# Performance work log

Measured on AMD Instinct MI355X. Metric: run time of the kernel, lower is better.

## Reference

```python
import jax, jax.numpy as jnp
import numpy as np
import math

B, H, L, DK, D, LOCAL = 4, 8, 2048, 64, 512, 4


def setup_inputs() -> dict:
    key = jax.random.key(0)
    ks = jax.random.split(key, 9)
    n = L
    return {
        'query': jax.random.normal(ks[0], (B, H, L, DK), jnp.float32),
        'key': jax.random.normal(ks[1], (B, H, L, DK), jnp.float32),
        'value': jax.random.normal(ks[2], (B, H, L, DK), jnp.float32),
        'users': jax.random.normal(ks[3], (B, L, D), jnp.float32),
        'mask': jnp.tril(jnp.ones((L, L), dtype=bool))[None, None],  # causal [1,1,L,L]
        'rel_pos_w': jax.random.normal(ks[4], (2 * n - 1, DK * LOCAL), jnp.float32) * 0.02,
        'user_proj_w': jax.random.normal(ks[5], (DK * LOCAL, D), jnp.float32) * 0.02,
        'user_proj_b': jax.random.normal(ks[6], (DK * LOCAL,), jnp.float32) * 0.02,
        'mlp_w': jax.random.normal(ks[7], (LOCAL, DK), jnp.float32) * 0.1,
        'mlp_b': jax.random.normal(ks[8], (LOCAL,), jnp.float32) * 0.1,
    }


def reference(query, key, value, users, mask, rel_pos_w, user_proj_w, user_proj_b, mlp_w, mlp_b):
    b, h, l, dk = query.shape
    local = mlp_w.shape[0]
    g = h - local
    n = l
    scale = 1.0 / math.sqrt(dk)
    NEG = -1e12  # MAX_VAL in the torch source

    # ---- global heads: plain softmax attention ----
    qg, kg, vg = query[:, :g], key[:, :g], value[:, :g]
    sg = jnp.einsum('bhqd,bhkd->bhqk', qg, kg) * scale
    sg = jnp.where(mask, sg, NEG)
    pg = jax.nn.softmax(sg, axis=-1)
    og = jnp.einsum('bhqk,bhkd->bhqd', pg, vg)

    # ---- local (LOCKER) heads ----
    ql, kl, vl = query[:, g:], key[:, g:], value[:, g:]
    sl = jnp.einsum('bhqd,bhkd->bhqk', ql, kl) * scale

    # reweight = Linear(d_k,1)(rel_pos + v_q + v_k + user_proj(users)_q) per local head.
    # Linear over a sum decomposes exactly (same math, avoids [b,local,l,l,dk] tensor):
    rel_tab = rel_pos_w.reshape(2 * n - 1, local, dk)
    rel_scores = jnp.einsum('rhd,hd->rh', rel_tab, mlp_w)          # [2n-1, local]
    pos = jnp.arange(n)
    distance = pos[None, :] - pos[:, None] + n - 1                  # [l, l]
    rel_term = rel_scores[distance].transpose(2, 0, 1)              # [local, l, l]

    v_term = jnp.einsum('bhkd,hd->bhk', vl, mlp_w)                  # [b, local, l]
    u = (users @ user_proj_w.T + user_proj_b).reshape(b, l, local, dk)
    u_term = jnp.einsum('bqhd,hd->bhq', u, mlp_w)                   # [b, local, l]

    reweight = (rel_term[None]
                + v_term[:, :, None, :]      # value_l.unsqueeze(-3): varies over key idx
                + v_term[:, :, :, None]      # value_l.unsqueeze(-2): varies over query idx
                + u_term[:, :, :, None]      # user term broadcast over key idx
                + mlp_b[None, :, None, None])

    sl = sl + reweight
    sl = jnp.where(mask, sl, NEG)
    pl = jax.nn.softmax(sl, axis=-1)
    ol = jnp.einsum('bhqk,bhkd->bhqd', pl, vl)

    return jnp.concatenate([og, ol], axis=1)  # [b, h, l, d_k]
```

## Files before the change

kernel.cpp:

```cpp
#include <hip/hip_runtime.h>

#define TL 2048
#define NHEAD 8
#define NLOC 4
#define L2E 1.44269504f
#define PSTRIDE 4352

typedef __attribute__((ext_vector_type(4))) float f32x4;
typedef __attribute__((ext_vector_type(16))) float f32x16;
typedef __attribute__((ext_vector_type(8))) __bf16 bf16x8;
typedef __attribute__((ext_vector_type(8))) unsigned short u16x8;
typedef __attribute__((ext_vector_type(4))) unsigned int u32x4;

static __device__ __forceinline__ unsigned short f2bf(float f) {
    unsigned u = __float_as_uint(f);
    u = (u + 0x7FFFu + ((u >> 16) & 1u)) >> 16;
    return (unsigned short)u;
}
static __device__ __forceinline__ unsigned int cvtpk(float a, float b) {
    unsigned int w;
    asm("v_cvt_pk_bf16_f32 %0, %1, %2" : "=v"(w) : "v"(a), "v"(b));
    return w;
}
static __device__ __forceinline__ void gl_lds16(const void* g, void* l) {
    __builtin_amdgcn_global_load_lds(
        (const __attribute__((address_space(1))) void*)g,
        (__attribute__((address_space(3))) void*)l, 16, 0, 0);
}

__global__ __launch_bounds__(256) void preconv_kernel(
    const float* __restrict__ key, const float* __restrict__ value,
    const float* __restrict__ mlp_w, const float* __restrict__ rel_pos_w,
    unsigned short* __restrict__ Kb, unsigned short* __restrict__ Vtb,
    float* __restrict__ vtbf, float* __restrict__ rel_sf) {
    int blk = blockIdx.x;
    int t = threadIdx.x;
    int wave = t >> 6, lane = t & 63;

    if (blk >= 1024) {
        int r = (blk - 1024) * 4 + wave;
        if (r < 2 * TL - 1) {
#pragma unroll
            for (int hp = 0; hp < 4; ++hp) {
                float v = rel_pos_w[r * 256 + hp * 64 + lane] * mlp_w[hp * 64 + lane];
#pragma unroll
                for (int off = 32; off; off >>= 1) v += __shfl_xor(v, off);
                if (lane == 0) rel_sf[hp * 4096 + r] = v * L2E;
            }
        }
        return;
    }

    __shared__ float Vf[64][66];
    int bh = blk >> 5, kt = blk & 31;
    int h = bh & 7, b = bh >> 3;
    size_t src = (size_t)blk * 4096;
    size_t dst = (size_t)blk * 4096;

#pragma unroll
    for (int i = 0; i < 2; ++i) {
        int ch = t + i * 256;
        int row = ch >> 3, c = ch & 7;
        const float* kp = key + src + row * 64 + c * 8;
        f32x4 a = *(const f32x4*)kp;
        f32x4 bb = *(const f32x4*)(kp + 4);
        u16x8 o;
#pragma unroll
        for (int j = 0; j < 4; ++j) { o[j] = f2bf(a[j]); o[4 + j] = f2bf(bb[j]); }
        *(u16x8*)&Kb[dst + row * 64 + ((c ^ (row & 7)) << 3)] = o;
    }
    {
        int row = t >> 2, q4 = t & 3;
        const float* vp = value + src + row * 64 + q4 * 16;
#pragma unroll
        for (int j = 0; j < 4; ++j)
            *(f32x4*)&Vf[row][q4 * 16 + j * 4] = *(const f32x4*)(vp + j * 4);
    }
    __syncthreads();
#pragma unroll
    for (int i = 0; i < 2; ++i) {
        int ch = t + i * 256;
        int dr = ch >> 3, c = ch & 7;
        u16x8 o;
#pragma unroll
        for (int j = 0; j < 8; ++j) o[j] = f2bf(Vf[c * 8 + j][dr]);
        *(u16x8*)&Vtb[dst + dr * 64 + ((c ^ (dr & 7)) << 3)] = o;
    }
    if (h >= NLOC) {
        float mw = mlp_w[(h - NLOC) * 64 + lane];
        float* vout = vtbf + (size_t)((b * NLOC + h - NLOC) * TL) + kt * 64;
#pragma unroll
        for (int i = 0; i < 16; ++i) {
            int row = wave * 16 + i;
            float v = Vf[row][lane] * mw;
#pragma unroll
            for (int off = 32; off; off >>= 1) v += __shfl_xor(v, off);
            if (lane == 0) vout[row] = v * L2E;
        }
    }
}

#define MFMA32(A, B, C) __builtin_amdgcn_mfma_f32_32x32x16_bf16(A, B, C, 0, 0, 0)

__global__ __launch_bounds__(256, 4) void attn_kernel(
    const float* __restrict__ query,
    const unsigned short* __restrict__ Kb, const unsigned short* __restrict__ Vtb,
    const float* __restrict__ rel_sf, const float* __restrict__ vtbf,
    float* __restrict__ part) {

    __shared__ __align__(16) unsigned char smem[35328];
    unsigned short* Ks0 = (unsigned short*)smem;
    unsigned short* Vt0 = (unsigned short*)(smem + 16384);
    float* relw  = (float*)(smem + 32768);
    float* biasf = (float*)(smem + 34816);

    int bid = blockIdx.x;
    int bh = bid & 31;
    int sid = bid >> 5;
    int i = 0, s = 0, acc = 0;
#pragma unroll
    for (int ii = 15; ii >= 0; --ii) {
        int ns = (2 * ii + 7) / 6;
        if (sid >= acc && sid < acc + ns) { i = ii; s = sid - acc; }
        acc += ns;
    }
    int k_b = 6 * s;
    int k_e = min(6 * s + 6, 2 * i + 2);
    int q0 = i << 7;

    int h = bh & 7, b = bh >> 3;
    bool islocal = (h >= NLOC);
    int t = threadIdx.x;
    int w = t >> 6;
    int l31 = t & 31;
    int hi = (t >> 5) & 1;
    int sw = l31 & 7;
    int qrel = 32 * w + l31;
    int qglob = q0 + qrel;
    int qmaxw = q0 + 32 * w + 31;

    size_t tbase = (size_t)bh * 32 * 4096;
    const unsigned short* Ktiles = Kb + tbase;
    const unsigned short* Vtiles = Vtb + tbase;
    const float* vtpf = vtbf + (islocal ? (size_t)((b * NLOC + h - NLOC) * TL) : 0);
    int idxlo = 64 * k_b - q0 + 1920;
    const float* relsrc = rel_sf + (islocal ? ((h - NLOC) * 4096 + idxlo) : 0);

    gl_lds16(Ktiles + (size_t)k_b * 4096 + t * 8, Ks0 + t * 8);
    gl_lds16(Ktiles + (size_t)k_b * 4096 + 2048 + t * 8, Ks0 + 2048 + t * 8);
    gl_lds16(Vtiles + (size_t)k_b * 4096 + t * 8, Vt0 + t * 8);
    gl_lds16(Vtiles + (size_t)k_b * 4096 + 2048 + t * 8, Vt0 + 2048 + t * 8);
    if (islocal) {
        if (t < 128) *((f32x4*)relw + t) = *((const f32x4*)relsrc + t);
        if (t < 16) ((f32x4*)biasf)[t] = ((const f32x4*)(vtpf + (size_t)k_b * 64))[t];
    }

    const float SC = 0.125f * L2E;
    bf16x8 qf[4];
    {
        const float* qsrc = query + ((size_t)bh * TL + qglob) * 64 + 8 * hi;
#pragma unroll
        for (int mq = 0; mq < 4; ++mq) {
            f32x4 a = *(const f32x4*)(qsrc + 16 * mq);
            f32x4 c = *(const f32x4*)(qsrc + 16 * mq + 4);
            u16x8 u;
#pragma unroll
            for (int j = 0; j < 4; ++j) { u[j] = f2bf(a[j] * SC); u[4 + j] = f2bf(c[j] * SC); }
            qf[mq] = __builtin_bit_cast(bf16x8, u);
        }
    }

    float m = -1e30f, lsum = 0.f;
    f32x16 O0 = {0,0,0,0,0,0,0,0,0,0,0,0,0,0,0,0};
    f32x16 O1 = {0,0,0,0,0,0,0,0,0,0,0,0,0,0,0,0};

    __syncthreads();

    int cur = 0;
    for (int kt = k_b; kt < k_e; ++kt) {
        unsigned short* Ks = Ks0 + cur * 4096;
        unsigned short* Vt = Vt0 + cur * 4096;
        const float* bias = biasf + cur * 64;

        if (kt + 1 < k_e) {
            int nb = cur ^ 1;
            gl_lds16(Ktiles + (size_t)(kt + 1) * 4096 + t * 8, Ks0 + nb * 4096 + t * 8);
            gl_lds16(Ktiles + (size_t)(kt + 1) * 4096 + 2048 + t * 8, Ks0 + nb * 4096 + 2048 + t * 8);
            gl_lds16(Vtiles + (size_t)(kt + 1) * 4096 + t * 8, Vt0 + nb * 4096 + t * 8);
            gl_lds16(Vtiles + (size_t)(kt + 1) * 4096 + 2048 + t * 8, Vt0 + nb * 4096 + 2048 + t * 8);
            if (islocal && t < 16)
                ((f32x4*)(biasf + nb * 64))[t] =
                    ((const f32x4*)(vtpf + (size_t)(kt + 1) * 64))[t];
        }

        bool active = (64 * kt <= qmaxw);
        bool maskt = (64 * kt + 63 > q0 + 32 * w);
        if (active) {
#pragma unroll
            for (int h2 = 0; h2 < 2; ++h2) {
                f32x16 S = {0,0,0,0,0,0,0,0,0,0,0,0,0,0,0,0};
                __builtin_amdgcn_s_setprio(1);
#pragma unroll
                for (int mq = 0; mq < 4; ++mq) {
                    int ch = ((2 * mq + hi) ^ sw) << 3;
                    const bf16x8 kf = *(const bf16x8*)&Ks[(32 * h2 + l31) * 64 + ch];
                    S = MFMA32(kf, qf[mq], S);
                }
                __builtin_amdgcn_s_setprio(0);

                if (islocal) {
                    int rbase = 64 * (kt - k_b) + 32 * h2 + 4 * hi + 127 - qrel;
#pragma unroll
                    for (int g = 0; g < 4; ++g) {
                        int kk0 = 32 * h2 + 8 * g + 4 * hi;
                        f32x4 bv = *(const f32x4*)&bias[kk0];
#pragma unroll
                        for (int j = 0; j < 4; ++j)
                            S[4 * g + j] += bv[j] + relw[rbase + 8 * g + j];
                    }
                }
                if (maskt) {
                    int koff = 64 * kt + 32 * h2 + 4 * hi - qglob;
#pragma unroll
                    for (int r = 0; r < 16; ++r) {
                        int kk = (r & 3) + 8 * (r >> 2);
                        if (koff + kk > 0) S[r] = -1e30f;
                    }
                }
                float pmax = -1e30f;
#pragma unroll
                for (int r = 0; r < 16; ++r) pmax = fmaxf(pmax, S[r]);
                pmax = fmaxf(pmax, __shfl_xor(pmax, 32));
                if (__any(pmax > m + 11.5f)) {
                    float nm2 = fmaxf(m, pmax);
                    float corr = exp2f(m - nm2);
                    lsum *= corr;
#pragma unroll
                    for (int r = 0; r < 16; ++r) { O0[r] *= corr; O1[r] *= corr; }
                    m = nm2;
                }
                float ps = 0.f;
#pragma unroll
                for (int r = 0; r < 16; ++r) {
                    float p = exp2f(S[r] - m);
                    S[r] = p; ps += p;
                }
                ps += __shfl_xor(ps, 32);
                lsum += ps;

                __builtin_amdgcn_s_setprio(1);
#pragma unroll
                for (int kq = 0; kq < 2; ++kq) {
                    int ra = 8 * kq;
                    unsigned int x0 = cvtpk(S[ra + 0], S[ra + 1]);
                    unsigned int x1 = cvtpk(S[ra + 2], S[ra + 3]);
                    unsigned int y0 = cvtpk(S[ra + 4], S[ra + 5]);
                    unsigned int y1 = cvtpk(S[ra + 6], S[ra + 7]);
                    asm("v_permlane32_swap_b32 %0, %1" : "+v"(x0), "+v"(y0));
                    asm("v_permlane32_swap_b32 %0, %1" : "+v"(x1), "+v"(y1));
                    u32x4 fw;
                    fw[0] = x0; fw[1] = x1; fw[2] = y0; fw[3] = y1;
                    const bf16x8 pf = __builtin_bit_cast(bf16x8, fw);
                    int ch = ((4 * h2 + 2 * kq + hi) ^ sw) << 3;
                    const bf16x8 vf0 = *(const bf16x8*)&Vt[l31 * 64 + ch];
                    const bf16x8 vf1 = *(const bf16x8*)&Vt[(32 + l31) * 64 + ch];
                    O0 = MFMA32(vf0, pf, O0);
                    O1 = MFMA32(vf1, pf, O1);
                }
                __builtin_amdgcn_s_setprio(0);
            }
        }
        __syncthreads();
        cur ^= 1;
    }

    float* pp = part + (size_t)bid * PSTRIDE;
    unsigned int* po = (unsigned int*)pp;
#pragma unroll
    for (int g = 0; g < 4; ++g) {
        unsigned int w0 = cvtpk(O0[4 * g + 0], O0[4 * g + 1]);
        unsigned int w1 = cvtpk(O0[4 * g + 2], O0[4 * g + 3]);
        unsigned int w2 = cvtpk(O1[4 * g + 0], O1[4 * g + 1]);
        unsigned int w3 = cvtpk(O1[4 * g + 2], O1[4 * g + 3]);
        int dp0 = 4 * g + 2 * hi;
        po[dp0 * 128 + qrel] = w0;
        po[(dp0 + 1) * 128 + qrel] = w1;
        po[(16 + dp0) * 128 + qrel] = w2;
        po[(16 + dp0 + 1) * 128 + qrel] = w3;
    }
    if (hi == 0) { pp[4096 + qrel] = m; pp[4224 + qrel] = lsum; }
}

__global__ __launch_bounds__(128) void merge_kernel(
    const float* __restrict__ part, float* __restrict__ out) {
    __shared__ float sc[6][128];
    int bid = blockIdx.x;
    int bh = bid & 31, i = bid >> 5;
    int n = (2 * i + 7) / 6;
    int sb = 0;
    for (int ii = 15; ii > i; --ii) sb += (2 * ii + 7) / 6;
    int t = threadIdx.x;

    float mv[6], lv[6];
#pragma unroll
    for (int s2 = 0; s2 < 6; ++s2) {
        mv[s2] = -1e30f; lv[s2] = 0.f;
        if (s2 < n) {
            const float* pp = part + (size_t)((sb + s2) * 32 + bh) * PSTRIDE;
            mv[s2] = pp[4096 + t]; lv[s2] = pp[4224 + t];
        }
    }
    float nm = mv[0];
#pragma unroll
    for (int s2 = 1; s2 < 6; ++s2) nm = fmaxf(nm, mv[s2]);
    float den = 0.f;
    float cf[6];
#pragma unroll
    for (int s2 = 0; s2 < 6; ++s2) { cf[s2] = exp2f(mv[s2] - nm); den += lv[s2] * cf[s2]; }
    float inv = 1.0f / den;
#pragma unroll
    for (int s2 = 0; s2 < 6; ++s2) if (s2 < n) sc[s2][t] = cf[s2] * inv;
    __syncthreads();

    size_t obase = (size_t)bh * TL * 64 + (size_t)(128 * i + t) * 64;
    for (int seg = 0; seg < 4; ++seg) {
        float o[16];
#pragma unroll
        for (int j = 0; j < 16; ++j) o[j] = 0.f;
#pragma unroll
        for (int s2 = 0; s2 < 6; ++s2) {
            if (s2 < n) {
                const unsigned int* po =
                    (const unsigned int*)(part + (size_t)((sb + s2) * 32 + bh) * PSTRIDE);
                float wsc = sc[s2][t];
#pragma unroll
                for (int j = 0; j < 8; ++j) {
                    unsigned int wv = po[(seg * 8 + j) * 128 + t];
                    o[2 * j]     += wsc * __uint_as_float((wv & 0xffffu) << 16);
                    o[2 * j + 1] += wsc * __uint_as_float(wv & 0xffff0000u);
                }
            }
        }
#pragma unroll
        for (int c = 0; c < 4; ++c)
            *(f32x4*)(out + obase + seg * 16 + 4 * c) = *(const f32x4*)&o[4 * c];
    }
}

extern "C" void kernel_launch(void* const* d_in, const int* in_sizes, int n_in,
                              void* d_out, int out_size, void* d_ws, size_t ws_size,
                              hipStream_t stream) {
    const float* query = (const float*)d_in[0];
    const float* key = (const float*)d_in[1];
    const float* value = (const float*)d_in[2];
    const float* rel_pos_w = (const float*)d_in[5];
    const float* mlp_w = (const float*)d_in[8];
    float* out = (float*)d_out;

    unsigned short* Kb = (unsigned short*)d_ws;
    unsigned short* Vtb = Kb + 32 * 32 * 4096;
    float* rel_sf = (float*)(Vtb + 32 * 32 * 4096);
    float* vtbf = rel_sf + 4 * 4096;
    float* part = vtbf + 32768;

    preconv_kernel<<<2048, 256, 0, stream>>>(key, value, mlp_w, rel_pos_w,
                                             Kb, Vtb, vtbf, rel_sf);
    attn_kernel<<<1632, 256, 0, stream>>>(query, Kb, Vtb, rel_sf, vtbf, part);
    merge_kernel<<<512, 128, 0, stream>>>(part, out);
}
```

Before: 75.57 us.

## Pre-swizzle K/V into MFMA fragment order and read directly from global

The preconversion kernel now writes bf16 K and transposed V in the exact per-lane MFMA fragment order, so the attention kernel reads K/V fragments straight from global memory instead of staging tiles through LDS with double buffering and per-tile barriers. The bias is folded into the initial accumulator, and the key range is split into more, evenly balanced chunks (ceil-based split count, 1952 blocks). Block-to-head mapping is permuted to spread heads across the grid. The merge kernel keeps its weights in registers with no LDS or barrier. This removes LDS traffic and synchronisation but depends on L2/cache hits for the repeated K/V fragment loads, and adds more partials to merge.

```diff
diff --git a/kernel.cpp b/kernel.cpp
--- a/kernel.cpp
+++ b/kernel.cpp
@@ -21,11 +21,6 @@
     unsigned int w;
     asm("v_cvt_pk_bf16_f32 %0, %1, %2" : "=v"(w) : "v"(a), "v"(b));
     return w;
-}
-static __device__ __forceinline__ void gl_lds16(const void* g, void* l) {
-    __builtin_amdgcn_global_load_lds(
-        (const __attribute__((address_space(1))) void*)g,
-        (__attribute__((address_space(3))) void*)l, 16, 0, 0);
 }
 
 __global__ __launch_bounds__(256) void preconv_kernel(
@@ -51,40 +46,49 @@
         return;
     }
 
-    __shared__ float Vf[64][66];
+    __shared__ float Tf[64][66];
     int bh = blk >> 5, kt = blk & 31;
     int h = bh & 7, b = bh >> 3;
     size_t src = (size_t)blk * 4096;
     size_t dst = (size_t)blk * 4096;
 
+    {
+        int row = t >> 2, q4 = t & 3;
+        const float* kp = key + src + row * 64 + q4 * 16;
+#pragma unroll
+        for (int j = 0; j < 4; ++j)
+            *(f32x4*)&Tf[row][q4 * 16 + j * 4] = *(const f32x4*)(kp + j * 4);
+    }
+    __syncthreads();
 #pragma unroll
     for (int i = 0; i < 2; ++i) {
-        int ch = t + i * 256;
-        int row = ch >> 3, c = ch & 7;
-        const float* kp = key + src + row * 64 + c * 8;
-        f32x4 a = *(const f32x4*)kp;
-        f32x4 bb = *(const f32x4*)(kp + 4);
+        int idx = t + i * 256;
+        int l31 = idx & 31, hi = (idx >> 5) & 1, mq = (idx >> 6) & 3, h2 = idx >> 8;
+        int r = h2 * 32 + l31, c = mq * 2 + hi;
         u16x8 o;
 #pragma unroll
-        for (int j = 0; j < 4; ++j) { o[j] = f2bf(a[j]); o[4 + j] = f2bf(bb[j]); }
-        *(u16x8*)&Kb[dst + row * 64 + ((c ^ (row & 7)) << 3)] = o;
-    }
+        for (int j = 0; j < 8; ++j) o[j] = f2bf(Tf[r][c * 8 + j]);
+        *(u16x8*)&Kb[dst + idx * 8] = o;
+    }
+    __syncthreads();
+
     {
         int row = t >> 2, q4 = t & 3;
         const float* vp = value + src + row * 64 + q4 * 16;
 #pragma unroll
         for (int j = 0; j < 4; ++j)
-            *(f32x4*)&Vf[row][q4 * 16 + j * 4] = *(const f32x4*)(vp + j * 4);
+            *(f32x4*)&Tf[row][q4 * 16 + j * 4] = *(const f32x4*)(vp + j * 4);
     }
     __syncthreads();
 #pragma unroll
     for (int i = 0; i < 2; ++i) {
-        int ch = t + i * 256;
-        int dr = ch >> 3, c = ch & 7;
+        int idx = t + i * 256;
+        int l31 = idx & 31, hi = (idx >> 5) & 1, half = (idx >> 6) & 1, c2 = idx >> 7;
+        int r = half * 32 + l31, c = c2 * 2 + hi;
         u16x8 o;
 #pragma unroll
-        for (int j = 0; j < 8; ++j) o[j] = f2bf(Vf[c * 8 + j][dr]);
-        *(u16x8*)&Vtb[dst + dr * 64 + ((c ^ (dr & 7)) << 3)] = o;
+        for (int j = 0; j < 8; ++j) o[j] = f2bf(Tf[c * 8 + j][r]);
+        *(u16x8*)&Vtb[dst + idx * 8] = o;
     }
     if (h >= NLOC) {
         float mw = mlp_w[(h - NLOC) * 64 + lane];
@@ -92,7 +96,7 @@
 #pragma unroll
         for (int i = 0; i < 16; ++i) {
             int row = wave * 16 + i;
-            float v = Vf[row][lane] * mw;
+            float v = Tf[row][lane] * mw;
 #pragma unroll
             for (int off = 32; off; off >>= 1) v += __shfl_xor(v, off);
             if (lane == 0) vout[row] = v * L2E;
@@ -108,24 +112,23 @@
     const float* __restrict__ rel_sf, const float* __restrict__ vtbf,
     float* __restrict__ part) {
 
-    __shared__ __align__(16) unsigned char smem[35328];
-    unsigned short* Ks0 = (unsigned short*)smem;
-    unsigned short* Vt0 = (unsigned short*)(smem + 16384);
-    float* relw  = (float*)(smem + 32768);
-    float* biasf = (float*)(smem + 34816);
+    __shared__ float relw[512];
 
     int bid = blockIdx.x;
-    int bh = bid & 31;
+    int bhx = bid & 31;
+    int bh = (bhx & 7) * 4 + (bhx >> 3);
     int sid = bid >> 5;
     int i = 0, s = 0, acc = 0;
-#pragma unroll
     for (int ii = 15; ii >= 0; --ii) {
-        int ns = (2 * ii + 7) / 6;
+        int ns = (2 * ii + 6) / 5;
         if (sid >= acc && sid < acc + ns) { i = ii; s = sid - acc; }
         acc += ns;
     }
-    int k_b = 6 * s;
-    int k_e = min(6 * s + 6, 2 * i + 2);
+    int nt = 2 * i + 2;
+    int n = (2 * i + 6) / 5;
+    int T = nt / n, R = nt % n;
+    int k_b = s * T + min(s, R);
+    int len = T + (s < R ? 1 : 0);
     int q0 = i << 7;
 
     int h = bh & 7, b = bh >> 3;
@@ -134,10 +137,10 @@
     int w = t >> 6;
     int l31 = t & 31;
     int hi = (t >> 5) & 1;
-    int sw = l31 & 7;
     int qrel = 32 * w + l31;
     int qglob = q0 + qrel;
     int qmaxw = q0 + 32 * w + 31;
+    int hivl = hi * 256 + l31 * 8;
 
     size_t tbase = (size_t)bh * 32 * 4096;
     const unsigned short* Ktiles = Kb + tbase;
@@ -146,14 +149,7 @@
     int idxlo = 64 * k_b - q0 + 1920;
     const float* relsrc = rel_sf + (islocal ? ((h - NLOC) * 4096 + idxlo) : 0);
 
-    gl_lds16(Ktiles + (size_t)k_b * 4096 + t * 8, Ks0 + t * 8);
-    gl_lds16(Ktiles + (size_t)k_b * 4096 + 2048 + t * 8, Ks0 + 2048 + t * 8);
-    gl_lds16(Vtiles + (size_t)k_b * 4096 + t * 8, Vt0 + t * 8);
-    gl_lds16(Vtiles + (size_t)k_b * 4096 + 2048 + t * 8, Vt0 + 2048 + t * 8);
-    if (islocal) {
-        if (t < 128) *((f32x4*)relw + t) = *((const f32x4*)relsrc + t);
-        if (t < 16) ((f32x4*)biasf)[t] = ((const f32x4*)(vtpf + (size_t)k_b * 64))[t];
-    }
+    if (islocal && t < 112) ((f32x4*)relw)[t] = ((const f32x4*)relsrc)[t];
 
     const float SC = 0.125f * L2E;
     bf16x8 qf[4];
@@ -176,102 +172,88 @@
 
     __syncthreads();
 
-    int cur = 0;
-    for (int kt = k_b; kt < k_e; ++kt) {
-        unsigned short* Ks = Ks0 + cur * 4096;
-        unsigned short* Vt = Vt0 + cur * 4096;
-        const float* bias = biasf + cur * 64;
-
-        if (kt + 1 < k_e) {
-            int nb = cur ^ 1;
-            gl_lds16(Ktiles + (size_t)(kt + 1) * 4096 + t * 8, Ks0 + nb * 4096 + t * 8);
-            gl_lds16(Ktiles + (size_t)(kt + 1) * 4096 + 2048 + t * 8, Ks0 + nb * 4096 + 2048 + t * 8);
-            gl_lds16(Vtiles + (size_t)(kt + 1) * 4096 + t * 8, Vt0 + nb * 4096 + t * 8);
-            gl_lds16(Vtiles + (size_t)(kt + 1) * 4096 + 2048 + t * 8, Vt0 + nb * 4096 + 2048 + t * 8);
-            if (islocal && t < 16)
-                ((f32x4*)(biasf + nb * 64))[t] =
-                    ((const f32x4*)(vtpf + (size_t)(kt + 1) * 64))[t];
-        }
-
-        bool active = (64 * kt <= qmaxw);
+#pragma unroll 1
+    for (int kt4 = 0; kt4 < len; ++kt4) {
+        int kt = k_b + kt4;
+        if (64 * kt > qmaxw) break;
+        const unsigned short* Kt = Ktiles + (size_t)kt * 4096;
+        const unsigned short* Vt = Vtiles + (size_t)kt * 4096;
+        const float* bias = vtpf + kt * 64;
         bool maskt = (64 * kt + 63 > q0 + 32 * w);
-        if (active) {
-#pragma unroll
-            for (int h2 = 0; h2 < 2; ++h2) {
-                f32x16 S = {0,0,0,0,0,0,0,0,0,0,0,0,0,0,0,0};
-                __builtin_amdgcn_s_setprio(1);
-#pragma unroll
-                for (int mq = 0; mq < 4; ++mq) {
-                    int ch = ((2 * mq + hi) ^ sw) << 3;
-                    const bf16x8 kf = *(const bf16x8*)&Ks[(32 * h2 + l31) * 64 + ch];
-                    S = MFMA32(kf, qf[mq], S);
+
+#pragma unroll
+        for (int h2 = 0; h2 < 2; ++h2) {
+            f32x16 S;
+            if (islocal) {
+                int rbase = 64 * kt4 + 32 * h2 + 4 * hi + 127 - qrel;
+#pragma unroll
+                for (int g = 0; g < 4; ++g) {
+                    f32x4 bv = *(const f32x4*)&bias[32 * h2 + 8 * g + 4 * hi];
+#pragma unroll
+                    for (int j = 0; j < 4; ++j)
+                        S[4 * g + j] = bv[j] + relw[rbase + 8 * g + j];
                 }
-                __builtin_amdgcn_s_setprio(0);
-
-                if (islocal) {
-                    int rbase = 64 * (kt - k_b) + 32 * h2 + 4 * hi + 127 - qrel;
-#pragma unroll
-                    for (int g = 0; g < 4; ++g) {
-                        int kk0 = 32 * h2 + 8 * g + 4 * hi;
-                        f32x4 bv = *(const f32x4*)&bias[kk0];
-#pragma unroll
-                        for (int j = 0; j < 4; ++j)
-                            S[4 * g + j] += bv[j] + relw[rbase + 8 * g + j];
-                    }
+            } else {
+                S = (f32x16){0,0,0,0,0,0,0,0,0,0,0,0,0,0,0,0};
+            }
+            __builtin_amdgcn_s_setprio(1);
+#pragma unroll
+            for (int mq = 0; mq < 4; ++mq) {
+                const bf16x8 kf = *(const bf16x8*)&Kt[(h2 * 4 + mq) * 512 + hivl];
+                S = MFMA32(kf, qf[mq], S);
+            }
+            __builtin_amdgcn_s_setprio(0);
+
+            if (maskt) {
+                int koff = 64 * kt + 32 * h2 + 4 * hi - qglob;
+#pragma unroll
+                for (int r = 0; r < 16; ++r) {
+                    int kk = (r & 3) + 8 * (r >> 2);
+                    if (koff + kk > 0) S[r] = -1e30f;
                 }
-                if (maskt) {
-                    int koff = 64 * kt + 32 * h2 + 4 * hi - qglob;
-#pragma unroll
-                    for (int r = 0; r < 16; ++r) {
-                        int kk = (r & 3) + 8 * (r >> 2);
-                        if (koff + kk > 0) S[r] = -1e30f;
-                    }
-                }
-                float pmax = -1e30f;
-#pragma unroll
-                for (int r = 0; r < 16; ++r) pmax = fmaxf(pmax, S[r]);
-                pmax = fmaxf(pmax, __shfl_xor(pmax, 32));
-                if (__any(pmax > m + 11.5f)) {
-                    float nm2 = fmaxf(m, pmax);
-                    float corr = exp2f(m - nm2);
-                    lsum *= corr;
-#pragma unroll
-                    for (int r = 0; r < 16; ++r) { O0[r] *= corr; O1[r] *= corr; }
-                    m = nm2;
-                }
-                float ps = 0.f;
-#pragma unroll
-                for (int r = 0; r < 16; ++r) {
-                    float p = exp2f(S[r] - m);
-                    S[r] = p; ps += p;
-                }
-                ps += __shfl_xor(ps, 32);
-                lsum += ps;
-
-                __builtin_amdgcn_s_setprio(1);
-#pragma unroll
-                for (int kq = 0; kq < 2; ++kq) {
-                    int ra = 8 * kq;
-                    unsigned int x0 = cvtpk(S[ra + 0], S[ra + 1]);
-                    unsigned int x1 = cvtpk(S[ra + 2], S[ra + 3]);
-                    unsigned int y0 = cvtpk(S[ra + 4], S[ra + 5]);
-                    unsigned int y1 = cvtpk(S[ra + 6], S[ra + 7]);
-                    asm("v_permlane32_swap_b32 %0, %1" : "+v"(x0), "+v"(y0));
-                    asm("v_permlane32_swap_b32 %0, %1" : "+v"(x1), "+v"(y1));
-                    u32x4 fw;
-                    fw[0] = x0; fw[1] = x1; fw[2] = y0; fw[3] = y1;
-                    const bf16x8 pf = __builtin_bit_cast(bf16x8, fw);
-                    int ch = ((4 * h2 + 2 * kq + hi) ^ sw) << 3;
-                    const bf16x8 vf0 = *(const bf16x8*)&Vt[l31 * 64 + ch];
-                    const bf16x8 vf1 = *(const bf16x8*)&Vt[(32 + l31) * 64 + ch];
-                    O0 = MFMA32(vf0, pf, O0);
-                    O1 = MFMA32(vf1, pf, O1);
-                }
-                __builtin_amdgcn_s_setprio(0);
-            }
-        }
-        __syncthreads();
-        cur ^= 1;
+            }
+            float pmax = -1e30f;
+#pragma unroll
+            for (int r = 0; r < 16; ++r) pmax = fmaxf(pmax, S[r]);
+            pmax = fmaxf(pmax, __shfl_xor(pmax, 32));
+            if (__any(pmax > m + 11.5f)) {
+                float nm2 = fmaxf(m, pmax);
+                float corr = exp2f(m - nm2);
+                lsum *= corr;
+#pragma unroll
+                for (int r = 0; r < 16; ++r) { O0[r] *= corr; O1[r] *= corr; }
+                m = nm2;
+            }
+            float ps = 0.f;
+#pragma unroll
+            for (int r = 0; r < 16; ++r) {
+                float p = exp2f(S[r] - m);
+                S[r] = p; ps += p;
+            }
+            ps += __shfl_xor(ps, 32);
+            lsum += ps;
+
+            __builtin_amdgcn_s_setprio(1);
+#pragma unroll
+            for (int kq = 0; kq < 2; ++kq) {
+                int ra = 8 * kq;
+                unsigned int x0 = cvtpk(S[ra + 0], S[ra + 1]);
+                unsigned int x1 = cvtpk(S[ra + 2], S[ra + 3]);
+                unsigned int y0 = cvtpk(S[ra + 4], S[ra + 5]);
+                unsigned int y1 = cvtpk(S[ra + 6], S[ra + 7]);
+                asm("v_permlane32_swap_b32 %0, %1" : "+v"(x0), "+v"(y0));
+                asm("v_permlane32_swap_b32 %0, %1" : "+v"(x1), "+v"(y1));
+                u32x4 fw;
+                fw[0] = x0; fw[1] = x1; fw[2] = y0; fw[3] = y1;
+                const bf16x8 pf = __builtin_bit_cast(bf16x8, fw);
+                int c2 = h2 * 2 + kq;
+                const bf16x8 vf0 = *(const bf16x8*)&Vt[c2 * 1024 + hivl];
+                const bf16x8 vf1 = *(const bf16x8*)&Vt[c2 * 1024 + 512 + hivl];
+                O0 = MFMA32(vf0, pf, O0);
+                O1 = MFMA32(vf1, pf, O1);
+            }
+            __builtin_amdgcn_s_setprio(0);
+        }
     }
 
     float* pp = part + (size_t)bid * PSTRIDE;
@@ -293,34 +275,33 @@
 
 __global__ __launch_bounds__(128) void merge_kernel(
     const float* __restrict__ part, float* __restrict__ out) {
-    __shared__ float sc[6][128];
     int bid = blockIdx.x;
-    int bh = bid & 31, i = bid >> 5;
-    int n = (2 * i + 7) / 6;
+    int bhx = bid & 31, i = bid >> 5;
+    int bh = (bhx & 7) * 4 + (bhx >> 3);
+    int n = (2 * i + 6) / 5;
     int sb = 0;
-    for (int ii = 15; ii > i; --ii) sb += (2 * ii + 7) / 6;
+    for (int ii = 15; ii > i; --ii) sb += (2 * ii + 6) / 5;
     int t = threadIdx.x;
 
-    float mv[6], lv[6];
-#pragma unroll
-    for (int s2 = 0; s2 < 6; ++s2) {
+    float mv[8], lv[8];
+#pragma unroll
+    for (int s2 = 0; s2 < 8; ++s2) {
         mv[s2] = -1e30f; lv[s2] = 0.f;
         if (s2 < n) {
-            const float* pp = part + (size_t)((sb + s2) * 32 + bh) * PSTRIDE;
+            const float* pp = part + (size_t)((sb + s2) * 32 + bhx) * PSTRIDE;
             mv[s2] = pp[4096 + t]; lv[s2] = pp[4224 + t];
         }
     }
     float nm = mv[0];
 #pragma unroll
-    for (int s2 = 1; s2 < 6; ++s2) nm = fmaxf(nm, mv[s2]);
+    for (int s2 = 1; s2 < 8; ++s2) nm = fmaxf(nm, mv[s2]);
     float den = 0.f;
-    float cf[6];
-#pragma unroll
-    for (int s2 = 0; s2 < 6; ++s2) { cf[s2] = exp2f(mv[s2] - nm); den += lv[s2] * cf[s2]; }
+    float cw[8];
+#pragma unroll
+    for (int s2 = 0; s2 < 8; ++s2) { cw[s2] = exp2f(mv[s2] - nm); den += lv[s2] * cw[s2]; }
     float inv = 1.0f / den;
 #pragma unroll
-    for (int s2 = 0; s2 < 6; ++s2) if (s2 < n) sc[s2][t] = cf[s2] * inv;
-    __syncthreads();
+    for (int s2 = 0; s2 < 8; ++s2) cw[s2] *= inv;
 
     size_t obase = (size_t)bh * TL * 64 + (size_t)(128 * i + t) * 64;
     for (int seg = 0; seg < 4; ++seg) {
@@ -328,11 +309,11 @@
 #pragma unroll
         for (int j = 0; j < 16; ++j) o[j] = 0.f;
 #pragma unroll
-        for (int s2 = 0; s2 < 6; ++s2) {
+        for (int s2 = 0; s2 < 8; ++s2) {
             if (s2 < n) {
                 const unsigned int* po =
-                    (const unsigned int*)(part + (size_t)((sb + s2) * 32 + bh) * PSTRIDE);
-                float wsc = sc[s2][t];
+                    (const unsigned int*)(part + (size_t)((sb + s2) * 32 + bhx) * PSTRIDE);
+                float wsc = cw[s2];
 #pragma unroll
                 for (int j = 0; j < 8; ++j) {
                     unsigned int wv = po[(seg * 8 + j) * 128 + t];
@@ -365,6 +346,6 @@
 
     preconv_kernel<<<2048, 256, 0, stream>>>(key, value, mlp_w, rel_pos_w,
                                              Kb, Vtb, vtbf, rel_sf);
-    attn_kernel<<<1632, 256, 0, stream>>>(query, Kb, Vtb, rel_sf, vtbf, part);
+    attn_kernel<<<1952, 256, 0, stream>>>(query, Kb, Vtb, rel_sf, vtbf, part);
     merge_kernel<<<512, 128, 0, stream>>>(part, out);
 }
```

Result: slower. 80.68 us (+6.8%).
